# Optimization experiments

Hardware: AMD Instinct MI355X
Metric: run time of the kernel (lower is better)

## Reference

```python
import jax, jax.numpy as jnp
import numpy as np

B, C, D, S = 4096, 256, 512, 8


def setup_inputs() -> dict:
    key = jax.random.key(0)
    k1, k2, k3, k4 = jax.random.split(key, 4)
    scale = 1.0 / np.sqrt(C)
    x = jax.random.normal(k1, (B, C), dtype=jnp.float32)
    subjects = jax.random.randint(k2, (B,), 0, S, dtype=jnp.int32)
    weights = jax.random.normal(k3, (S, C, D), dtype=jnp.float32) * scale  # (S,C,D)
    bias = jax.random.normal(k4, (S, D), dtype=jnp.float32) * scale       # (S,D)
    return {"x": x, "subjects": subjects, "weights": weights, "bias": bias}


def reference(x, subjects, weights, bias):
    # Per-sample weight gather: (B, C, D), faithful to torch index_select + einsum
    w = jnp.take(weights, subjects, axis=0)          # (B,C,D)
    out = jnp.einsum('bc,bcd->bd', x, w)             # (B,D)
    out = out + jnp.take(bias, subjects, axis=0)     # (B,D)
    return out
```

## Files before the change

kernel.cpp:

```cpp
#include <hip/hip_runtime.h>
#include <hip/hip_bf16.h>

#define BB 4096
#define CC 256
#define DD 512
#define SS 8

#define BM 64
#define BN 64
#define BK 64

typedef __attribute__((ext_vector_type(4))) float f32x4;
typedef __attribute__((ext_vector_type(8))) short s16x8;

static __device__ inline short f2bf(float f) {
    __hip_bfloat16 h = __float2bfloat16(f);
    return *reinterpret_cast<short*>(&h);
}

__global__ __launch_bounds__(256) void fused_kernel(
    const float* __restrict__ x, const int* __restrict__ subj,
    const float* __restrict__ w, const float* __restrict__ bias,
    float* __restrict__ out)
{
    const int s  = blockIdx.x & 7;
    const int rt = (blockIdx.x >> 3) & 15;
    const int ct = blockIdx.x >> 7;
    const int tid = threadIdx.x;
    const int lane = tid & 63, wv = tid >> 6;
    const unsigned long long lt = (1ull << lane) - 1ull;

    __shared__ __align__(16) short As[2][BM * BK];
    __shared__ __align__(16) short Bs[2][BK / 8][BN][8];
    __shared__ int wcnt[16][4];
    __shared__ int pre[16][4];
    __shared__ int rows_l[BM];
    __shared__ int ns_sh;

    if (tid < BM) rows_l[tid] = -1;

    int sl[16];
#pragma unroll
    for (int i = 0; i < 16; ++i) sl[i] = subj[tid + i * 256];
#pragma unroll
    for (int i = 0; i < 16; ++i) {
        unsigned long long m = __ballot(sl[i] == s);
        if (lane == 0) wcnt[i][wv] = __popcll(m);
    }
    __syncthreads();

    if (tid < 64) {
        int c = wcnt[tid >> 2][tid & 3];
        int inc = c;
#pragma unroll
        for (int d2 = 1; d2 < 64; d2 <<= 1) {
            int o = __shfl_up(inc, d2, 64);
            if (lane >= d2) inc += o;
        }
        pre[tid >> 2][tid & 3] = inc - c;
        if (tid == 63) ns_sh = inc;
    }
    __syncthreads();

    const int n_s = ns_sh;
    if (rt * BM >= n_s) return;
    int m_valid = n_s - rt * BM; if (m_valid > BM) m_valid = BM;

#pragma unroll
    for (int i = 0; i < 16; ++i) {
        unsigned long long m = __ballot(sl[i] == s);
        if (sl[i] == s) {
            int rank = pre[i][wv] + __popcll(m & lt);
            int p = rank - rt * BM;
            if (p >= 0 && p < BM) rows_l[p] = tid + i * 256;
        }
    }
    __syncthreads();

    const int wm = wv & 1, wn = wv >> 1;
    const int lr = lane & 15, lg = lane >> 4;

    f32x4 acc[2][2];
#pragma unroll
    for (int mf = 0; mf < 2; ++mf)
#pragma unroll
        for (int nf = 0; nf < 2; ++nf)
            acc[mf][nf] = (f32x4)0.0f;

    const int ar = tid >> 2;
    const int grow = rows_l[ar];
    const float* xp = x + (size_t)(grow < 0 ? 0 : grow) * CC + (tid & 3) * 16;
    const float* wb = w + (size_t)s * CC * DD + ct * BN + lane;

    f32x4 xa[4];
    float wf[2][8];

    auto LOADS = [&](int ks) {
        if (grow >= 0) {
#pragma unroll
            for (int i = 0; i < 4; ++i)
                xa[i] = *reinterpret_cast<const f32x4*>(xp + ks * BK + i * 4);
        } else {
#pragma unroll
            for (int i = 0; i < 4; ++i) xa[i] = (f32x4)0.0f;
        }
#pragma unroll
        for (int i = 0; i < 2; ++i) {
            int kb = wv + i * 4;
#pragma unroll
            for (int e = 0; e < 8; ++e)
                wf[i][e] = wb[(size_t)(ks * BK + kb * 8 + e) * DD];
        }
    };
    auto STORE = [&](int pb) {
#pragma unroll
        for (int i = 0; i < 2; ++i) {
            s16x8 p;
            p[0] = f2bf(xa[2 * i][0]); p[1] = f2bf(xa[2 * i][1]);
            p[2] = f2bf(xa[2 * i][2]); p[3] = f2bf(xa[2 * i][3]);
            p[4] = f2bf(xa[2 * i + 1][0]); p[5] = f2bf(xa[2 * i + 1][1]);
            p[6] = f2bf(xa[2 * i + 1][2]); p[7] = f2bf(xa[2 * i + 1][3]);
            int c = (tid & 3) * 2 + i;
            *reinterpret_cast<s16x8*>(reinterpret_cast<char*>(As[pb])
                + ar * 128 + ((c * 16) ^ ((ar & 7) << 4))) = p;
        }
#pragma unroll
        for (int i = 0; i < 2; ++i) {
            s16x8 p;
#pragma unroll
            for (int e = 0; e < 8; ++e) p[e] = f2bf(wf[i][e]);
            *reinterpret_cast<s16x8*>(&Bs[pb][wv + i * 4][lane][0]) = p;
        }
    };
    auto COMPUTE = [&](int pb) {
        s16x8 af[2][2], bfr[2][2];
#pragma unroll
        for (int mf = 0; mf < 2; ++mf) {
            int row = wm * 32 + mf * 16 + lr;
#pragma unroll
            for (int kh = 0; kh < 2; ++kh) {
                int kf2 = (kh * 32 + lg * 8) * 2;
                af[mf][kh] = *reinterpret_cast<s16x8*>(reinterpret_cast<char*>(As[pb])
                    + row * 128 + (kf2 ^ ((row & 7) << 4)));
            }
        }
#pragma unroll
        for (int nf = 0; nf < 2; ++nf) {
            int n = wn * 32 + nf * 16 + lr;
#pragma unroll
            for (int kh = 0; kh < 2; ++kh)
                bfr[nf][kh] = *reinterpret_cast<s16x8*>(&Bs[pb][kh * 4 + lg][n][0]);
        }
#pragma unroll
        for (int mf = 0; mf < 2; ++mf)
#pragma unroll
            for (int nf = 0; nf < 2; ++nf)
#pragma unroll
                for (int kh = 0; kh < 2; ++kh)
                    acc[mf][nf] = __builtin_amdgcn_mfma_f32_16x16x32_bf16(
                        af[mf][kh], bfr[nf][kh], acc[mf][nf], 0, 0, 0);
    };

    LOADS(0);
    STORE(0);
    __syncthreads();
#pragma unroll
    for (int ks = 0; ks < CC / BK - 1; ++ks) {
        LOADS(ks + 1);
        COMPUTE(ks & 1);
        STORE((ks + 1) & 1);
        __syncthreads();
    }
    COMPUTE((CC / BK - 1) & 1);

#pragma unroll
    for (int nf = 0; nf < 2; ++nf) {
        int col = ct * BN + wn * 32 + nf * 16 + lr;
        float bv = bias[s * DD + col];
#pragma unroll
        for (int mf = 0; mf < 2; ++mf) {
            int rl0 = wm * 32 + mf * 16 + lg * 4;
#pragma unroll
            for (int r = 0; r < 4; ++r) {
                int rl = rl0 + r;
                if (rl < m_valid) {
                    int g = rows_l[rl];
                    out[(size_t)g * DD + col] = acc[mf][nf][r] + bv;
                }
            }
        }
    }
}

extern "C" void kernel_launch(void* const* d_in, const int* in_sizes, int n_in,
                              void* d_out, int out_size, void* d_ws, size_t ws_size,
                              hipStream_t stream) {
    const float* x        = (const float*)d_in[0];
    const int*   subjects = (const int*)d_in[1];
    const float* weights  = (const float*)d_in[2];
    const float* bias     = (const float*)d_in[3];
    float* out = (float*)d_out;

    fused_kernel<<<1024, 256, 0, stream>>>(x, subjects, weights, bias, out);
}
```

Baseline: 17.86 us.

## Load A fragments directly into registers, bypass LDS, prefetch weights early

The x tile no longer goes through shared memory. Each lane reads its MFMA A-fragment straight from global memory, converts it to bf16 in registers and double-buffers it there. The first weight tile load is issued before the subject-compaction prologue, and bias is loaded before the main loop, so global latency overlaps the ballot and scan work. This removes LDS stores and reads and halves LDS use. The cost is more register pressure, and x is now read redundantly with narrower per-lane accesses, since the fragments from the two wave columns overlap.

```diff
diff --git a/kernel.cpp b/kernel.cpp
--- a/kernel.cpp
+++ b/kernel.cpp
@@ -30,12 +30,24 @@
     const int lane = tid & 63, wv = tid >> 6;
     const unsigned long long lt = (1ull << lane) - 1ull;
 
-    __shared__ __align__(16) short As[2][BM * BK];
     __shared__ __align__(16) short Bs[2][BK / 8][BN][8];
     __shared__ int wcnt[16][4];
     __shared__ int pre[16][4];
     __shared__ int rows_l[BM];
     __shared__ int ns_sh;
+
+    const float* wb = w + (size_t)s * CC * DD + ct * BN + lane;
+    float wf[2][8];
+    auto BLOAD = [&](int ks) {
+#pragma unroll
+        for (int i = 0; i < 2; ++i) {
+            int kb = wv + i * 4;
+#pragma unroll
+            for (int e = 0; e < 8; ++e)
+                wf[i][e] = wb[(size_t)(ks * BK + kb * 8 + e) * DD];
+        }
+    };
+    BLOAD(0);
 
     if (tid < BM) rows_l[tid] = -1;
 
@@ -80,6 +92,19 @@
     const int wm = wv & 1, wn = wv >> 1;
     const int lr = lane & 15, lg = lane >> 4;
 
+    float bv[2];
+#pragma unroll
+    for (int nf = 0; nf < 2; ++nf)
+        bv[nf] = bias[s * DD + ct * BN + wn * 32 + nf * 16 + lr];
+
+    int rla[2];
+    const float* xb[2];
+#pragma unroll
+    for (int mf = 0; mf < 2; ++mf) {
+        rla[mf] = rows_l[wm * 32 + mf * 16 + lr];
+        xb[mf] = x + (size_t)(rla[mf] < 0 ? 0 : rla[mf]) * CC + lg * 8;
+    }
+
     f32x4 acc[2][2];
 #pragma unroll
     for (int mf = 0; mf < 2; ++mf)
@@ -87,63 +112,33 @@
         for (int nf = 0; nf < 2; ++nf)
             acc[mf][nf] = (f32x4)0.0f;
 
-    const int ar = tid >> 2;
-    const int grow = rows_l[ar];
-    const float* xp = x + (size_t)(grow < 0 ? 0 : grow) * CC + (tid & 3) * 16;
-    const float* wb = w + (size_t)s * CC * DD + ct * BN + lane;
-
-    f32x4 xa[4];
-    float wf[2][8];
-
-    auto LOADS = [&](int ks) {
-        if (grow >= 0) {
-#pragma unroll
-            for (int i = 0; i < 4; ++i)
-                xa[i] = *reinterpret_cast<const f32x4*>(xp + ks * BK + i * 4);
-        } else {
-#pragma unroll
-            for (int i = 0; i < 4; ++i) xa[i] = (f32x4)0.0f;
-        }
-#pragma unroll
-        for (int i = 0; i < 2; ++i) {
-            int kb = wv + i * 4;
-#pragma unroll
-            for (int e = 0; e < 8; ++e)
-                wf[i][e] = wb[(size_t)(ks * BK + kb * 8 + e) * DD];
-        }
-    };
-    auto STORE = [&](int pb) {
+    s16x8 af[2][2][2];
+    auto ALOADCVT = [&](int ks, int pb) {
+#pragma unroll
+        for (int mf = 0; mf < 2; ++mf) {
+#pragma unroll
+            for (int kh = 0; kh < 2; ++kh) {
+                f32x4 v0 = *reinterpret_cast<const f32x4*>(xb[mf] + ks * BK + kh * 32);
+                f32x4 v1 = *reinterpret_cast<const f32x4*>(xb[mf] + ks * BK + kh * 32 + 4);
+                s16x8 p;
+                p[0] = f2bf(v0[0]); p[1] = f2bf(v0[1]); p[2] = f2bf(v0[2]); p[3] = f2bf(v0[3]);
+                p[4] = f2bf(v1[0]); p[5] = f2bf(v1[1]); p[6] = f2bf(v1[2]); p[7] = f2bf(v1[3]);
+                if (rla[mf] < 0) p = (s16x8)(short)0;
+                af[pb][mf][kh] = p;
+            }
+        }
+    };
+    auto BSTORE = [&](int pb) {
 #pragma unroll
         for (int i = 0; i < 2; ++i) {
             s16x8 p;
-            p[0] = f2bf(xa[2 * i][0]); p[1] = f2bf(xa[2 * i][1]);
-            p[2] = f2bf(xa[2 * i][2]); p[3] = f2bf(xa[2 * i][3]);
-            p[4] = f2bf(xa[2 * i + 1][0]); p[5] = f2bf(xa[2 * i + 1][1]);
-            p[6] = f2bf(xa[2 * i + 1][2]); p[7] = f2bf(xa[2 * i + 1][3]);
-            int c = (tid & 3) * 2 + i;
-            *reinterpret_cast<s16x8*>(reinterpret_cast<char*>(As[pb])
-                + ar * 128 + ((c * 16) ^ ((ar & 7) << 4))) = p;
-        }
-#pragma unroll
-        for (int i = 0; i < 2; ++i) {
-            s16x8 p;
 #pragma unroll
             for (int e = 0; e < 8; ++e) p[e] = f2bf(wf[i][e]);
             *reinterpret_cast<s16x8*>(&Bs[pb][wv + i * 4][lane][0]) = p;
         }
     };
-    auto COMPUTE = [&](int pb) {
-        s16x8 af[2][2], bfr[2][2];
-#pragma unroll
-        for (int mf = 0; mf < 2; ++mf) {
-            int row = wm * 32 + mf * 16 + lr;
-#pragma unroll
-            for (int kh = 0; kh < 2; ++kh) {
-                int kf2 = (kh * 32 + lg * 8) * 2;
-                af[mf][kh] = *reinterpret_cast<s16x8*>(reinterpret_cast<char*>(As[pb])
-                    + row * 128 + (kf2 ^ ((row & 7) << 4)));
-            }
-        }
+    auto COMPUTE = [&](int ks, int pb) {
+        s16x8 bfr[2][2];
 #pragma unroll
         for (int nf = 0; nf < 2; ++nf) {
             int n = wn * 32 + nf * 16 + lr;
@@ -158,25 +153,29 @@
 #pragma unroll
                 for (int kh = 0; kh < 2; ++kh)
                     acc[mf][nf] = __builtin_amdgcn_mfma_f32_16x16x32_bf16(
-                        af[mf][kh], bfr[nf][kh], acc[mf][nf], 0, 0, 0);
-    };
-
-    LOADS(0);
-    STORE(0);
-    __syncthreads();
-#pragma unroll
-    for (int ks = 0; ks < CC / BK - 1; ++ks) {
-        LOADS(ks + 1);
-        COMPUTE(ks & 1);
-        STORE((ks + 1) & 1);
-        __syncthreads();
-    }
-    COMPUTE((CC / BK - 1) & 1);
+                        af[pb][mf][kh], bfr[nf][kh], acc[mf][nf], 0, 0, 0);
+    };
+
+    ALOADCVT(0, 0);
+    BSTORE(0);
+    __syncthreads();
+
+#pragma unroll
+    for (int ks = 0; ks < CC / BK; ++ks) {
+        if (ks < CC / BK - 1) {
+            BLOAD(ks + 1);
+            ALOADCVT(ks + 1, (ks + 1) & 1);
+        }
+        COMPUTE(ks, ks & 1);
+        if (ks < CC / BK - 1) {
+            BSTORE((ks + 1) & 1);
+            __syncthreads();
+        }
+    }
 
 #pragma unroll
     for (int nf = 0; nf < 2; ++nf) {
         int col = ct * BN + wn * 32 + nf * 16 + lr;
-        float bv = bias[s * DD + col];
 #pragma unroll
         for (int mf = 0; mf < 2; ++mf) {
             int rl0 = wm * 32 + mf * 16 + lg * 4;
@@ -185,7 +184,7 @@
                 int rl = rl0 + r;
                 if (rl < m_valid) {
                     int g = rows_l[rl];
-                    out[(size_t)g * DD + col] = acc[mf][nf][r] + bv;
+                    out[(size_t)g * DD + col] = acc[mf][nf][r] + bv[nf];
                 }
             }
         }
```

After: 26.21 us. +46.7%, slower.
